# Optimization experiments

Measured on AMD Instinct MI355X. Metric: run time of the kernel, lower is better.

The kernel has to match this reference:

```python
import jax, jax.numpy as jnp
import numpy as np

N_NODES = 50000
N_EDGES = 600000
D_IN = 128
H = D_IN // 2  # 64
N_GRAPHS = 500
DIM_TARGET = 1


def setup_inputs() -> dict:
    key = jax.random.key(0)
    ks = jax.random.split(key, 16)
    x = jax.random.normal(ks[0], (N_NODES, D_IN), dtype=jnp.float32)
    edge_index = jax.random.randint(ks[1], (2, N_EDGES), 0, N_NODES, dtype=jnp.int64)
    batch = jnp.sort(jax.random.randint(ks[2], (N_NODES,), 0, N_GRAPHS, dtype=jnp.int64))
    # SAGEConv params: lin_l (neighbor aggregate, with bias), lin_r (root, no bias)
    s = 1.0 / np.sqrt(D_IN)
    Wl = jax.random.uniform(ks[3], (D_IN, H), jnp.float32, -s, s)
    bl = jnp.zeros((H,), jnp.float32)
    Wr = jax.random.uniform(ks[4], (D_IN, H), jnp.float32, -s, s)
    # MLP: 64->32->16->8->1
    dims = [H, H // 2, H // 4, H // 8, DIM_TARGET]
    params = {}
    for i in range(4):
        si = 1.0 / np.sqrt(dims[i])
        params[f"W{i}"] = jax.random.uniform(ks[5 + 2 * i], (dims[i], dims[i + 1]), jnp.float32, -si, si)
        params[f"b{i}"] = jax.random.uniform(ks[6 + 2 * i], (dims[i + 1],), jnp.float32, -si, si)
    return dict(x=x, edge_index=edge_index, batch=batch, Wl=Wl, bl=bl, Wr=Wr, **params)


def reference(x, edge_index, batch, Wl, bl, Wr, W0, b0, W1, b1, W2, b2, W3, b3):
    n_nodes = x.shape[0]
    src, dst = edge_index[0], edge_index[1]
    # SAGEConv mean aggregation: mean of source-node features at each target node
    agg = jax.ops.segment_sum(x[src], dst, num_segments=n_nodes)          # [N, D]
    cnt = jax.ops.segment_sum(jnp.ones((src.shape[0],), x.dtype), dst, num_segments=n_nodes)
    mean_nbr = agg / jnp.maximum(cnt, 1.0)[:, None]
    x1 = mean_nbr @ Wl + bl + x @ Wr                                      # [N, H]
    # global_mean_pool by graph id
    gsum = jax.ops.segment_sum(x1, batch, num_segments=N_GRAPHS)          # [G, H]
    gcnt = jax.ops.segment_sum(jnp.ones((n_nodes,), x.dtype), batch, num_segments=N_GRAPHS)
    h = gsum / jnp.maximum(gcnt, 1.0)[:, None]
    # MLP (dropout is identity in eval mode)
    h = jax.nn.relu(h @ W0 + b0)
    h = jax.nn.relu(h @ W1 + b1)
    h = jax.nn.relu(h @ W2 + b2)
    return h @ W3 + b3
```

## Files before the change

kernel.cpp:

```cpp
#include <hip/hip_runtime.h>
#include <hip/hip_bf16.h>

#define N_NODES  50000
#define N_EDGES  600000
#define D_IN     128
#define H        64
#define N_GRAPHS 500
#define MAXDEG   48

#define CONV_BLOCKS 6250
#define SCAT_CHUNKS 64
#define SCAT_BLOCKS 512
#define EDGES_PER_CHUNK (N_EDGES / SCAT_CHUNKS)
#define NODES_PER_SHARD (N_NODES / 8)
#define GST_BLOCKS  2
#define SPLIT       8

__device__ __forceinline__ float bflo(unsigned int u) { return __uint_as_float(u << 16); }
__device__ __forceinline__ float bfhi(unsigned int u) { return __uint_as_float(u & 0xffff0000u); }

__global__ __launch_bounds__(256) void prep_kernel(
        const float* __restrict__ x, unsigned short* __restrict__ xb,
        const int* __restrict__ src, const int* __restrict__ dst,
        int* __restrict__ deg, unsigned short* __restrict__ col,
        const int* __restrict__ batch, int* __restrict__ gstart) {
    int bid = blockIdx.x;
    if (bid < CONV_BLOCKS) {
        int i = bid * 256 + threadIdx.x;
        float4 f = ((const float4*)x)[i];
        ushort4 u;
        u.x = __bfloat16_as_ushort(__float2bfloat16(f.x));
        u.y = __bfloat16_as_ushort(__float2bfloat16(f.y));
        u.z = __bfloat16_as_ushort(__float2bfloat16(f.z));
        u.w = __bfloat16_as_ushort(__float2bfloat16(f.w));
        ((ushort4*)xb)[i] = u;
    } else if (bid < CONV_BLOCKS + SCAT_BLOCKS) {
        int rel   = bid - CONV_BLOCKS;
        int shard = bid & 7;
        int chunk = rel >> 3;
        int lo = shard * NODES_PER_SHARD;
        int hi = lo + NODES_PER_SHARD;
        int e0 = chunk * EDGES_PER_CHUNK;
        int e1 = e0 + EDGES_PER_CHUNK;
        for (int e = e0 + threadIdx.x; e < e1; e += 256) {
            int d = dst[e];
            if (d >= lo && d < hi) {
                int pos = atomicAdd(&deg[d], 1);
                if (pos < MAXDEG)
                    col[(size_t)d * MAXDEG + pos] = (unsigned short)src[e];
            }
        }
    } else {
        int g = (bid - CONV_BLOCKS - SCAT_BLOCKS) * 256 + threadIdx.x;
        if (g <= N_GRAPHS) {
            int lo = 0, hi = N_NODES;
            while (lo < hi) {
                int m = (lo + hi) >> 1;
                if (batch[m] < g) lo = m + 1; else hi = m;
            }
            gstart[g] = lo;
        }
    }
}

__global__ __launch_bounds__(256) void gather_kernel(
        const unsigned short* __restrict__ xb, const unsigned short* __restrict__ col,
        const int* __restrict__ deg, const int* __restrict__ batch,
        const int* __restrict__ gstart,
        float* __restrict__ Pn, float* __restrict__ Px, int* __restrict__ gcnt) {
    __shared__ float red[4 * D_IN];
    int bid  = blockIdx.x;
    int wave = threadIdx.x >> 6;
    int lane = threadIdx.x & 63;

    if (bid < N_GRAPHS * SPLIT) {
        int g = bid >> 3;
        int s = bid & 7;
        int n0 = gstart[g], n1 = gstart[g + 1];
        const unsigned short* xl = xb + 2 * lane;

        float2 pn = make_float2(0.f, 0.f);
        for (int n = n0 + s * 4 + wave; n < n1; n += 4 * SPLIT) {
            int d = deg[n];
            int dl = (d < MAXDEG) ? d : MAXDEG;
            const unsigned short* cl = col + (size_t)n * MAXDEG;
            int cidx = (lane < dl) ? (int)cl[lane] : 0;

            float2 t = make_float2(0.f, 0.f);
            int j = 0;
            for (; j + 8 <= dl; j += 8) {
                int s0 = __shfl(cidx, j),     s1 = __shfl(cidx, j + 1);
                int s2 = __shfl(cidx, j + 2), s3 = __shfl(cidx, j + 3);
                int s4 = __shfl(cidx, j + 4), s5 = __shfl(cidx, j + 5);
                int s6 = __shfl(cidx, j + 6), s7 = __shfl(cidx, j + 7);
                unsigned int u0 = *(const unsigned int*)(xl + (size_t)s0 * D_IN);
                unsigned int u1 = *(const unsigned int*)(xl + (size_t)s1 * D_IN);
                unsigned int u2 = *(const unsigned int*)(xl + (size_t)s2 * D_IN);
                unsigned int u3 = *(const unsigned int*)(xl + (size_t)s3 * D_IN);
                unsigned int u4 = *(const unsigned int*)(xl + (size_t)s4 * D_IN);
                unsigned int u5 = *(const unsigned int*)(xl + (size_t)s5 * D_IN);
                unsigned int u6 = *(const unsigned int*)(xl + (size_t)s6 * D_IN);
                unsigned int u7 = *(const unsigned int*)(xl + (size_t)s7 * D_IN);
                t.x += bflo(u0) + bflo(u1) + bflo(u2) + bflo(u3)
                     + bflo(u4) + bflo(u5) + bflo(u6) + bflo(u7);
                t.y += bfhi(u0) + bfhi(u1) + bfhi(u2) + bfhi(u3)
                     + bfhi(u4) + bfhi(u5) + bfhi(u6) + bfhi(u7);
            }
            for (; j + 4 <= dl; j += 4) {
                int s0 = __shfl(cidx, j),     s1 = __shfl(cidx, j + 1);
                int s2 = __shfl(cidx, j + 2), s3 = __shfl(cidx, j + 3);
                unsigned int u0 = *(const unsigned int*)(xl + (size_t)s0 * D_IN);
                unsigned int u1 = *(const unsigned int*)(xl + (size_t)s1 * D_IN);
                unsigned int u2 = *(const unsigned int*)(xl + (size_t)s2 * D_IN);
                unsigned int u3 = *(const unsigned int*)(xl + (size_t)s3 * D_IN);
                t.x += bflo(u0) + bflo(u1) + bflo(u2) + bflo(u3);
                t.y += bfhi(u0) + bfhi(u1) + bfhi(u2) + bfhi(u3);
            }
            for (; j < dl; ++j) {
                int sn = __shfl(cidx, j);
                unsigned int u = *(const unsigned int*)(xl + (size_t)sn * D_IN);
                t.x += bflo(u); t.y += bfhi(u);
            }
            if (d > 0) {
                float w = __builtin_amdgcn_rcpf((float)d);
                pn.x = fmaf(t.x, w, pn.x);
                pn.y = fmaf(t.y, w, pn.y);
            }
        }
        red[wave * D_IN + 2 * lane]     = pn.x;
        red[wave * D_IN + 2 * lane + 1] = pn.y;
        __syncthreads();
        if (threadIdx.x < D_IN) {
            float v = red[threadIdx.x] + red[D_IN + threadIdx.x]
                    + red[2 * D_IN + threadIdx.x] + red[3 * D_IN + threadIdx.x];
            atomicAdd(&Pn[g * D_IN + threadIdx.x], v);
        }
    } else {
        int p  = bid - N_GRAPHS * SPLIT;
        int n0 = gstart[p], n1 = gstart[p + 1];
        float fx = 0.f, fy = 0.f;
        for (int n = n0 + wave; n < n1; n += 4) {
            unsigned int u = *(const unsigned int*)(xb + (size_t)n * D_IN + 2 * lane);
            fx += bflo(u); fy += bfhi(u);
        }
        red[wave * D_IN + 2 * lane]     = fx;
        red[wave * D_IN + 2 * lane + 1] = fy;
        __syncthreads();
        if (threadIdx.x < D_IN) {
            float v = red[threadIdx.x] + red[D_IN + threadIdx.x]
                    + red[2 * D_IN + threadIdx.x] + red[3 * D_IN + threadIdx.x];
            Px[p * D_IN + threadIdx.x] = v;
        }
        if (threadIdx.x == 0) gcnt[p] = n1 - n0;
    }
}

__global__ void final_kernel(
        const float* __restrict__ Pn, const float* __restrict__ Px,
        const int* __restrict__ gcnt,
        const float* __restrict__ Wl, const float* __restrict__ bl,
        const float* __restrict__ Wr,
        const float* __restrict__ W0, const float* __restrict__ b0,
        const float* __restrict__ W1, const float* __restrict__ b1,
        const float* __restrict__ W2, const float* __restrict__ b2,
        const float* __restrict__ W3, const float* __restrict__ b3,
        float* __restrict__ out) {
    int g = blockIdx.x;
    int t = threadIdx.x;
    __shared__ float sp[D_IN], sx[D_IN], h[H], a0[32], a1[16], a2[8];
    sp[t]      = Pn[g * D_IN + t];
    sp[t + 64] = Pn[g * D_IN + 64 + t];
    sx[t]      = Px[g * D_IN + t];
    sx[t + 64] = Px[g * D_IN + 64 + t];
    __syncthreads();

    int ng = gcnt[g];
    float acc = 0.f;
    #pragma unroll 8
    for (int d = 0; d < D_IN; ++d)
        acc += sp[d] * Wl[d * H + t] + sx[d] * Wr[d * H + t];
    h[t] = (ng > 0) ? (acc / (float)ng + bl[t]) : 0.f;
    __syncthreads();

    if (t < 32) { float a = b0[t]; for (int d = 0; d < H;  ++d) a += h[d]  * W0[d * 32 + t]; a0[t] = fmaxf(a, 0.f); }
    __syncthreads();
    if (t < 16) { float a = b1[t]; for (int d = 0; d < 32; ++d) a += a0[d] * W1[d * 16 + t]; a1[t] = fmaxf(a, 0.f); }
    __syncthreads();
    if (t < 8)  { float a = b2[t]; for (int d = 0; d < 16; ++d) a += a1[d] * W2[d * 8 + t];  a2[t] = fmaxf(a, 0.f); }
    __syncthreads();
    if (t == 0) { float a = b3[0]; for (int d = 0; d < 8;  ++d) a += a2[d] * W3[d]; out[g] = a; }
}

extern "C" void kernel_launch(void* const* d_in, const int* in_sizes, int n_in,
                              void* d_out, int out_size, void* d_ws, size_t ws_size,
                              hipStream_t stream) {
    const float* x     = (const float*)d_in[0];
    const int*   ei    = (const int*)  d_in[1];
    const int*   batch = (const int*)  d_in[2];
    const float* Wl    = (const float*)d_in[3];
    const float* bl    = (const float*)d_in[4];
    const float* Wr    = (const float*)d_in[5];
    const float* W0    = (const float*)d_in[6];
    const float* b0    = (const float*)d_in[7];
    const float* W1    = (const float*)d_in[8];
    const float* b1    = (const float*)d_in[9];
    const float* W2    = (const float*)d_in[10];
    const float* b2    = (const float*)d_in[11];
    const float* W3    = (const float*)d_in[12];
    const float* b3    = (const float*)d_in[13];
    float* out = (float*)d_out;

    char* ws = (char*)d_ws;
    int*            deg    = (int*)(ws + 0);
    float*          Pn     = (float*)(ws + 200704);
    float*          Px     = (float*)(ws + 460800);
    int*            gcnt   = (int*)(ws + 716800);
    int*            gstart = (int*)(ws + 720896);
    unsigned short* col    = (unsigned short*)(ws + 724992);
    unsigned short* xb     = (unsigned short*)(ws + 5524992);

    hipMemsetAsync(ws, 0, 456704, stream);

    prep_kernel<<<CONV_BLOCKS + SCAT_BLOCKS + GST_BLOCKS, 256, 0, stream>>>(
        x, xb, ei, ei + N_EDGES, deg, col, batch, gstart);
    gather_kernel<<<N_GRAPHS * SPLIT + N_GRAPHS, 256, 0, stream>>>(
        xb, col, deg, batch, gstart, Pn, Px, gcnt);
    final_kernel<<<N_GRAPHS, 64, 0, stream>>>(Pn, Px, gcnt, Wl, bl, Wr,
                                              W0, b0, W1, b1, W2, b2, W3, b3, out);
}
```

Before: 180.7 us.

## Shard bf16 features into 8 column slices for cache-local neighbor gathers

The bf16 copy of x is reorganised into 8 contiguous slices of 16 features each, so every gather block touches only a 0.8 MB slice that can stay resident in L2. Each wave now gathers 8 neighbors at once, with 8 lanes per neighbor reading 32 bytes. Partial sums are combined with cross-lane shuffles. The grid grows to 8 slices times 4 sub-splits per graph, and the edge scatter uses more, smaller chunks. In exchange there are more blocks and atomics, and each neighbor row is loaded as short 32-byte segments rather than full rows.

```diff
diff --git a/kernel.cpp b/kernel.cpp
--- a/kernel.cpp
+++ b/kernel.cpp
@@ -8,41 +8,56 @@
 #define N_GRAPHS 500
 #define MAXDEG   48
 
-#define CONV_BLOCKS 6250
-#define SCAT_CHUNKS 64
-#define SCAT_BLOCKS 512
-#define EDGES_PER_CHUNK (N_EDGES / SCAT_CHUNKS)
-#define NODES_PER_SHARD (N_NODES / 8)
+#define NSH      8
+#define SLICE_U  (N_NODES * 8)
+
+#define CONV_BLOCKS 1563
+#define SCAT_CHUNKS 512
+#define SCAT_BLOCKS (SCAT_CHUNKS * 8)
+#define EPC         1172
+#define NPS         (N_NODES / 8)
 #define GST_BLOCKS  2
-#define SPLIT       8
+
+#define GSUB   4
+#define GMAIN  (N_GRAPHS * 8 * GSUB)
+#define PX_BLK (N_GRAPHS * 8)
 
 __device__ __forceinline__ float bflo(unsigned int u) { return __uint_as_float(u << 16); }
 __device__ __forceinline__ float bfhi(unsigned int u) { return __uint_as_float(u & 0xffff0000u); }
+__device__ __forceinline__ unsigned int packbf(float lo, float hi) {
+    unsigned int a = __bfloat16_as_ushort(__float2bfloat16(lo));
+    unsigned int b = __bfloat16_as_ushort(__float2bfloat16(hi));
+    return a | (b << 16);
+}
 
 __global__ __launch_bounds__(256) void prep_kernel(
-        const float* __restrict__ x, unsigned short* __restrict__ xb,
+        const float* __restrict__ x, unsigned int* __restrict__ xbs,
         const int* __restrict__ src, const int* __restrict__ dst,
         int* __restrict__ deg, unsigned short* __restrict__ col,
         const int* __restrict__ batch, int* __restrict__ gstart) {
-    int bid = blockIdx.x;
+    int bid = blockIdx.x, t = threadIdx.x;
     if (bid < CONV_BLOCKS) {
-        int i = bid * 256 + threadIdx.x;
-        float4 f = ((const float4*)x)[i];
-        ushort4 u;
-        u.x = __bfloat16_as_ushort(__float2bfloat16(f.x));
-        u.y = __bfloat16_as_ushort(__float2bfloat16(f.y));
-        u.z = __bfloat16_as_ushort(__float2bfloat16(f.z));
-        u.w = __bfloat16_as_ushort(__float2bfloat16(f.w));
-        ((ushort4*)xb)[i] = u;
+        int i = bid * 256 + t;
+        if (i < N_NODES * NSH) {
+            int node = i >> 3, s = i & 7;
+            const float4* xr = (const float4*)(x + (size_t)node * D_IN + s * 16);
+            float4 a = xr[0], b = xr[1], c = xr[2], d = xr[3];
+            uint4 o0, o1;
+            o0.x = packbf(a.x, a.y); o0.y = packbf(a.z, a.w);
+            o0.z = packbf(b.x, b.y); o0.w = packbf(b.z, b.w);
+            o1.x = packbf(c.x, c.y); o1.y = packbf(c.z, c.w);
+            o1.z = packbf(d.x, d.y); o1.w = packbf(d.z, d.w);
+            uint4* o = (uint4*)(xbs + (size_t)s * SLICE_U + node * 8);
+            o[0] = o0; o[1] = o1;
+        }
     } else if (bid < CONV_BLOCKS + SCAT_BLOCKS) {
         int rel   = bid - CONV_BLOCKS;
         int shard = bid & 7;
         int chunk = rel >> 3;
-        int lo = shard * NODES_PER_SHARD;
-        int hi = lo + NODES_PER_SHARD;
-        int e0 = chunk * EDGES_PER_CHUNK;
-        int e1 = e0 + EDGES_PER_CHUNK;
-        for (int e = e0 + threadIdx.x; e < e1; e += 256) {
+        int lo = shard * NPS, hi = lo + NPS;
+        int e0 = chunk * EPC;
+        int e1 = e0 + EPC; if (e1 > N_EDGES) e1 = N_EDGES;
+        for (int e = e0 + t; e < e1; e += 256) {
             int d = dst[e];
             if (d >= lo && d < hi) {
                 int pos = atomicAdd(&deg[d], 1);
@@ -51,7 +66,7 @@
             }
         }
     } else {
-        int g = (bid - CONV_BLOCKS - SCAT_BLOCKS) * 256 + threadIdx.x;
+        int g = (bid - CONV_BLOCKS - SCAT_BLOCKS) * 256 + t;
         if (g <= N_GRAPHS) {
             int lo = 0, hi = N_NODES;
             while (lo < hi) {
@@ -64,94 +79,68 @@
 }
 
 __global__ __launch_bounds__(256) void gather_kernel(
-        const unsigned short* __restrict__ xb, const unsigned short* __restrict__ col,
-        const int* __restrict__ deg, const int* __restrict__ batch,
-        const int* __restrict__ gstart,
+        const unsigned int* __restrict__ xbs, const unsigned short* __restrict__ col,
+        const int* __restrict__ deg, const int* __restrict__ gstart,
         float* __restrict__ Pn, float* __restrict__ Px, int* __restrict__ gcnt) {
-    __shared__ float red[4 * D_IN];
-    int bid  = blockIdx.x;
-    int wave = threadIdx.x >> 6;
-    int lane = threadIdx.x & 63;
-
-    if (bid < N_GRAPHS * SPLIT) {
-        int g = bid >> 3;
-        int s = bid & 7;
+    __shared__ float red[512];
+    int bid = blockIdx.x, t = threadIdx.x;
+    int wave = t >> 6, lane = t & 63;
+    int s  = bid & 7;
+    int sw = lane >> 3, pr = lane & 7;
+    const unsigned int* xs = xbs + (size_t)s * SLICE_U;
+
+    if (bid < GMAIN) {
+        int gi  = bid >> 3;
+        int g   = gi >> 2;
+        int sub = gi & 3;
         int n0 = gstart[g], n1 = gstart[g + 1];
-        const unsigned short* xl = xb + 2 * lane;
-
-        float2 pn = make_float2(0.f, 0.f);
-        for (int n = n0 + s * 4 + wave; n < n1; n += 4 * SPLIT) {
-            int d = deg[n];
+
+        float ax = 0.f, ay = 0.f;
+        for (int n = n0 + sub * 4 + wave; n < n1; n += 4 * GSUB) {
+            int d  = deg[n];
             int dl = (d < MAXDEG) ? d : MAXDEG;
-            const unsigned short* cl = col + (size_t)n * MAXDEG;
-            int cidx = (lane < dl) ? (int)cl[lane] : 0;
-
-            float2 t = make_float2(0.f, 0.f);
-            int j = 0;
-            for (; j + 8 <= dl; j += 8) {
-                int s0 = __shfl(cidx, j),     s1 = __shfl(cidx, j + 1);
-                int s2 = __shfl(cidx, j + 2), s3 = __shfl(cidx, j + 3);
-                int s4 = __shfl(cidx, j + 4), s5 = __shfl(cidx, j + 5);
-                int s6 = __shfl(cidx, j + 6), s7 = __shfl(cidx, j + 7);
-                unsigned int u0 = *(const unsigned int*)(xl + (size_t)s0 * D_IN);
-                unsigned int u1 = *(const unsigned int*)(xl + (size_t)s1 * D_IN);
-                unsigned int u2 = *(const unsigned int*)(xl + (size_t)s2 * D_IN);
-                unsigned int u3 = *(const unsigned int*)(xl + (size_t)s3 * D_IN);
-                unsigned int u4 = *(const unsigned int*)(xl + (size_t)s4 * D_IN);
-                unsigned int u5 = *(const unsigned int*)(xl + (size_t)s5 * D_IN);
-                unsigned int u6 = *(const unsigned int*)(xl + (size_t)s6 * D_IN);
-                unsigned int u7 = *(const unsigned int*)(xl + (size_t)s7 * D_IN);
-                t.x += bflo(u0) + bflo(u1) + bflo(u2) + bflo(u3)
-                     + bflo(u4) + bflo(u5) + bflo(u6) + bflo(u7);
-                t.y += bfhi(u0) + bfhi(u1) + bfhi(u2) + bfhi(u3)
-                     + bfhi(u4) + bfhi(u5) + bfhi(u6) + bfhi(u7);
-            }
-            for (; j + 4 <= dl; j += 4) {
-                int s0 = __shfl(cidx, j),     s1 = __shfl(cidx, j + 1);
-                int s2 = __shfl(cidx, j + 2), s3 = __shfl(cidx, j + 3);
-                unsigned int u0 = *(const unsigned int*)(xl + (size_t)s0 * D_IN);
-                unsigned int u1 = *(const unsigned int*)(xl + (size_t)s1 * D_IN);
-                unsigned int u2 = *(const unsigned int*)(xl + (size_t)s2 * D_IN);
-                unsigned int u3 = *(const unsigned int*)(xl + (size_t)s3 * D_IN);
-                t.x += bflo(u0) + bflo(u1) + bflo(u2) + bflo(u3);
-                t.y += bfhi(u0) + bfhi(u1) + bfhi(u2) + bfhi(u3);
-            }
-            for (; j < dl; ++j) {
-                int sn = __shfl(cidx, j);
-                unsigned int u = *(const unsigned int*)(xl + (size_t)sn * D_IN);
-                t.x += bflo(u); t.y += bfhi(u);
+            int cidx = (lane < dl) ? (int)col[(size_t)n * MAXDEG + lane] : 0;
+            float tx = 0.f, ty = 0.f;
+            for (int j = sw; j < dl; j += 8) {
+                int nb = __shfl(cidx, j);
+                unsigned int u = xs[nb * 8 + pr];
+                tx += bflo(u); ty += bfhi(u);
             }
             if (d > 0) {
                 float w = __builtin_amdgcn_rcpf((float)d);
-                pn.x = fmaf(t.x, w, pn.x);
-                pn.y = fmaf(t.y, w, pn.y);
-            }
-        }
-        red[wave * D_IN + 2 * lane]     = pn.x;
-        red[wave * D_IN + 2 * lane + 1] = pn.y;
+                ax = fmaf(tx, w, ax);
+                ay = fmaf(ty, w, ay);
+            }
+        }
+        ax += __shfl_xor(ax, 8); ax += __shfl_xor(ax, 16); ax += __shfl_xor(ax, 32);
+        ay += __shfl_xor(ay, 8); ay += __shfl_xor(ay, 16); ay += __shfl_xor(ay, 32);
+        if (lane < 8) { red[wave * 16 + 2 * pr] = ax; red[wave * 16 + 2 * pr + 1] = ay; }
         __syncthreads();
-        if (threadIdx.x < D_IN) {
-            float v = red[threadIdx.x] + red[D_IN + threadIdx.x]
-                    + red[2 * D_IN + threadIdx.x] + red[3 * D_IN + threadIdx.x];
-            atomicAdd(&Pn[g * D_IN + threadIdx.x], v);
+        if (t < 16) {
+            float v = red[t] + red[16 + t] + red[32 + t] + red[48 + t];
+            atomicAdd(&Pn[(size_t)g * D_IN + s * 16 + t], v);
         }
     } else {
-        int p  = bid - N_GRAPHS * SPLIT;
+        int p  = (bid - GMAIN) >> 3;
         int n0 = gstart[p], n1 = gstart[p + 1];
         float fx = 0.f, fy = 0.f;
-        for (int n = n0 + wave; n < n1; n += 4) {
-            unsigned int u = *(const unsigned int*)(xb + (size_t)n * D_IN + 2 * lane);
+        for (int n = n0 + (t >> 3); n < n1; n += 32) {
+            unsigned int u = xs[n * 8 + pr];
             fx += bflo(u); fy += bfhi(u);
         }
-        red[wave * D_IN + 2 * lane]     = fx;
-        red[wave * D_IN + 2 * lane + 1] = fy;
+        red[t] = fx; red[256 + t] = fy;
         __syncthreads();
-        if (threadIdx.x < D_IN) {
-            float v = red[threadIdx.x] + red[D_IN + threadIdx.x]
-                    + red[2 * D_IN + threadIdx.x] + red[3 * D_IN + threadIdx.x];
-            Px[p * D_IN + threadIdx.x] = v;
-        }
-        if (threadIdx.x == 0) gcnt[p] = n1 - n0;
+        if (t < 8) {
+            float v = 0.f;
+            for (int i = t; i < 256; i += 8) v += red[i];
+            Px[(size_t)p * D_IN + s * 16 + 2 * t] = v;
+        } else if (t < 16) {
+            int q = t - 8;
+            float v = 0.f;
+            for (int i = q; i < 256; i += 8) v += red[256 + i];
+            Px[(size_t)p * D_IN + s * 16 + 2 * q + 1] = v;
+        }
+        if (s == 0 && t == 0) gcnt[p] = n1 - n0;
     }
 }
 
@@ -213,18 +202,18 @@
     char* ws = (char*)d_ws;
     int*            deg    = (int*)(ws + 0);
     float*          Pn     = (float*)(ws + 200704);
-    float*          Px     = (float*)(ws + 460800);
-    int*            gcnt   = (int*)(ws + 716800);
-    int*            gstart = (int*)(ws + 720896);
-    unsigned short* col    = (unsigned short*)(ws + 724992);
-    unsigned short* xb     = (unsigned short*)(ws + 5524992);
+    int*            gstart = (int*)(ws + 458752);
+    unsigned short* col    = (unsigned short*)(ws + 460800);
+    unsigned int*   xbs    = (unsigned int*)(ws + 5261312);
+    float*          Px     = (float*)(ws + 18062336);
+    int*            gcnt   = (int*)(ws + 18318336);
 
     hipMemsetAsync(ws, 0, 456704, stream);
 
     prep_kernel<<<CONV_BLOCKS + SCAT_BLOCKS + GST_BLOCKS, 256, 0, stream>>>(
-        x, xb, ei, ei + N_EDGES, deg, col, batch, gstart);
-    gather_kernel<<<N_GRAPHS * SPLIT + N_GRAPHS, 256, 0, stream>>>(
-        xb, col, deg, batch, gstart, Pn, Px, gcnt);
+        x, xbs, ei, ei + N_EDGES, deg, col, batch, gstart);
+    gather_kernel<<<GMAIN + PX_BLK, 256, 0, stream>>>(
+        xbs, col, deg, gstart, Pn, Px, gcnt);
     final_kernel<<<N_GRAPHS, 64, 0, stream>>>(Pn, Px, gcnt, Wl, bl, Wr,
                                               W0, b0, W1, b1, W2, b2, W3, b3, out);
 }
```

After: 216.4 us. +19.8%, slower.

## Fuse prep, gather and MLP into one persistent kernel with grid barriers

Applied to the files above, without the earlier changes.

Replaces the memset plus three launches with a single 768-block persistent kernel. Stages are separated by atomic-counter grid barriers: zeroing the workspace, bf16 conversion and CSR scatter, per-graph gather, then the per-graph MLP. The root-feature sum now happens in the same wave loop as the neighbour gather, and partial sums go to global memory through per-lane atomics instead of a shared-memory reduction. This removes launch gaps and tail effects, but it relies on all 768 blocks being co-resident so the spin barriers do not deadlock, and it reduces parallelism in the conversion and scatter phases.

```diff
diff --git a/kernel.cpp b/kernel.cpp
--- a/kernel.cpp
+++ b/kernel.cpp
@@ -8,41 +8,92 @@
 #define N_GRAPHS 500
 #define MAXDEG   48
 
-#define CONV_BLOCKS 6250
-#define SCAT_CHUNKS 64
-#define SCAT_BLOCKS 512
-#define EDGES_PER_CHUNK (N_EDGES / SCAT_CHUNKS)
-#define NODES_PER_SHARD (N_NODES / 8)
-#define GST_BLOCKS  2
-#define SPLIT       8
+#define NBLK 768
+#define NTHR 256
+#define NW   (NBLK * NTHR)
+
+#define SCHUNKS 96
+#define EPC     (N_EDGES / SCHUNKS)
+#define NPS     (N_NODES / 8)
+
+#define GSUB   6
+#define GWAVES (N_GRAPHS * GSUB)
+
+#define OF_CTR  0
+#define OF_DEG  64
+#define OF_PN   200704
+#define OF_PX   456704
+#define OF_GST  712704
+#define OF_COL  716800
+#define OF_XB   5516800
+#define ZERO_Q  44540
 
 __device__ __forceinline__ float bflo(unsigned int u) { return __uint_as_float(u << 16); }
 __device__ __forceinline__ float bfhi(unsigned int u) { return __uint_as_float(u & 0xffff0000u); }
 
-__global__ __launch_bounds__(256) void prep_kernel(
-        const float* __restrict__ x, unsigned short* __restrict__ xb,
-        const int* __restrict__ src, const int* __restrict__ dst,
-        int* __restrict__ deg, unsigned short* __restrict__ col,
-        const int* __restrict__ batch, int* __restrict__ gstart) {
-    int bid = blockIdx.x;
-    if (bid < CONV_BLOCKS) {
-        int i = bid * 256 + threadIdx.x;
-        float4 f = ((const float4*)x)[i];
-        ushort4 u;
-        u.x = __bfloat16_as_ushort(__float2bfloat16(f.x));
-        u.y = __bfloat16_as_ushort(__float2bfloat16(f.y));
-        u.z = __bfloat16_as_ushort(__float2bfloat16(f.z));
-        u.w = __bfloat16_as_ushort(__float2bfloat16(f.w));
-        ((ushort4*)xb)[i] = u;
-    } else if (bid < CONV_BLOCKS + SCAT_BLOCKS) {
-        int rel   = bid - CONV_BLOCKS;
+__device__ __forceinline__ void gbar(int* ctr, int idx) {
+    __syncthreads();
+    if (threadIdx.x == 0) {
+        __threadfence();
+        __hip_atomic_fetch_add(&ctr[idx], 1, __ATOMIC_ACQ_REL, __HIP_MEMORY_SCOPE_AGENT);
+        while (__hip_atomic_load(&ctr[idx], __ATOMIC_ACQUIRE, __HIP_MEMORY_SCOPE_AGENT) < NBLK)
+            __builtin_amdgcn_s_sleep(1);
+        __threadfence();
+    }
+    __syncthreads();
+}
+
+__global__ __launch_bounds__(NTHR, 4) void gnn_kernel(
+        const float* __restrict__ x, const int* __restrict__ ei,
+        const int* __restrict__ batch,
+        const float* __restrict__ Wl, const float* __restrict__ bl,
+        const float* __restrict__ Wr,
+        const float* __restrict__ W0, const float* __restrict__ b0,
+        const float* __restrict__ W1, const float* __restrict__ b1,
+        const float* __restrict__ W2, const float* __restrict__ b2,
+        const float* __restrict__ W3, const float* __restrict__ b3,
+        char* __restrict__ ws, float* __restrict__ out) {
+    int* ctr             = (int*)(ws + OF_CTR);
+    int* deg             = (int*)(ws + OF_DEG);
+    float* Pn            = (float*)(ws + OF_PN);
+    float* Px            = (float*)(ws + OF_PX);
+    int* gstart          = (int*)(ws + OF_GST);
+    unsigned short* col  = (unsigned short*)(ws + OF_COL);
+    unsigned short* xb   = (unsigned short*)(ws + OF_XB);
+
+    int bid  = blockIdx.x, t = threadIdx.x;
+    int gtid = bid * NTHR + t;
+    int wave = t >> 6, lane = t & 63;
+
+    __shared__ float sp[D_IN], sx[D_IN], hs[H], a0[32], a1[16], a2[8];
+
+    const int* src = ei;
+    const int* dst = ei + N_EDGES;
+
+    {
+        uint4 z = make_uint4(0, 0, 0, 0);
+        uint4* zp = (uint4*)(ws + OF_DEG);
+        for (int i = gtid; i < ZERO_Q; i += NW) zp[i] = z;
+    }
+    gbar(ctr, 0);
+
+    {
+        const float4* xi = (const float4*)x;
+        ushort4* xo = (ushort4*)xb;
+        for (int i = gtid; i < N_NODES * D_IN / 4; i += NW) {
+            float4 f = xi[i];
+            ushort4 u;
+            u.x = __bfloat16_as_ushort(__float2bfloat16(f.x));
+            u.y = __bfloat16_as_ushort(__float2bfloat16(f.y));
+            u.z = __bfloat16_as_ushort(__float2bfloat16(f.z));
+            u.w = __bfloat16_as_ushort(__float2bfloat16(f.w));
+            xo[i] = u;
+        }
         int shard = bid & 7;
-        int chunk = rel >> 3;
-        int lo = shard * NODES_PER_SHARD;
-        int hi = lo + NODES_PER_SHARD;
-        int e0 = chunk * EDGES_PER_CHUNK;
-        int e1 = e0 + EDGES_PER_CHUNK;
-        for (int e = e0 + threadIdx.x; e < e1; e += 256) {
+        int chunk = bid >> 3;
+        int lo = shard * NPS, hi = lo + NPS;
+        int e0 = chunk * EPC, e1 = e0 + EPC;
+        for (int e = e0 + t; e < e1; e += NTHR) {
             int d = dst[e];
             if (d >= lo && d < hi) {
                 int pos = atomicAdd(&deg[d], 1);
@@ -50,145 +101,105 @@
                     col[(size_t)d * MAXDEG + pos] = (unsigned short)src[e];
             }
         }
-    } else {
-        int g = (bid - CONV_BLOCKS - SCAT_BLOCKS) * 256 + threadIdx.x;
-        if (g <= N_GRAPHS) {
-            int lo = 0, hi = N_NODES;
-            while (lo < hi) {
-                int m = (lo + hi) >> 1;
-                if (batch[m] < g) lo = m + 1; else hi = m;
+        if (bid >= NBLK - 8) {
+            int g = (bid - (NBLK - 8)) * NTHR + t;
+            if (g <= N_GRAPHS) {
+                int l = 0, h2 = N_NODES;
+                while (l < h2) { int m = (l + h2) >> 1; if (batch[m] < g) l = m + 1; else h2 = m; }
+                gstart[g] = l;
             }
-            gstart[g] = lo;
-        }
-    }
-}
-
-__global__ __launch_bounds__(256) void gather_kernel(
-        const unsigned short* __restrict__ xb, const unsigned short* __restrict__ col,
-        const int* __restrict__ deg, const int* __restrict__ batch,
-        const int* __restrict__ gstart,
-        float* __restrict__ Pn, float* __restrict__ Px, int* __restrict__ gcnt) {
-    __shared__ float red[4 * D_IN];
-    int bid  = blockIdx.x;
-    int wave = threadIdx.x >> 6;
-    int lane = threadIdx.x & 63;
-
-    if (bid < N_GRAPHS * SPLIT) {
-        int g = bid >> 3;
-        int s = bid & 7;
-        int n0 = gstart[g], n1 = gstart[g + 1];
-        const unsigned short* xl = xb + 2 * lane;
-
-        float2 pn = make_float2(0.f, 0.f);
-        for (int n = n0 + s * 4 + wave; n < n1; n += 4 * SPLIT) {
-            int d = deg[n];
-            int dl = (d < MAXDEG) ? d : MAXDEG;
-            const unsigned short* cl = col + (size_t)n * MAXDEG;
-            int cidx = (lane < dl) ? (int)cl[lane] : 0;
-
-            float2 t = make_float2(0.f, 0.f);
-            int j = 0;
-            for (; j + 8 <= dl; j += 8) {
-                int s0 = __shfl(cidx, j),     s1 = __shfl(cidx, j + 1);
-                int s2 = __shfl(cidx, j + 2), s3 = __shfl(cidx, j + 3);
-                int s4 = __shfl(cidx, j + 4), s5 = __shfl(cidx, j + 5);
-                int s6 = __shfl(cidx, j + 6), s7 = __shfl(cidx, j + 7);
-                unsigned int u0 = *(const unsigned int*)(xl + (size_t)s0 * D_IN);
-                unsigned int u1 = *(const unsigned int*)(xl + (size_t)s1 * D_IN);
-                unsigned int u2 = *(const unsigned int*)(xl + (size_t)s2 * D_IN);
-                unsigned int u3 = *(const unsigned int*)(xl + (size_t)s3 * D_IN);
-                unsigned int u4 = *(const unsigned int*)(xl + (size_t)s4 * D_IN);
-                unsigned int u5 = *(const unsigned int*)(xl + (size_t)s5 * D_IN);
-                unsigned int u6 = *(const unsigned int*)(xl + (size_t)s6 * D_IN);
-                unsigned int u7 = *(const unsigned int*)(xl + (size_t)s7 * D_IN);
-                t.x += bflo(u0) + bflo(u1) + bflo(u2) + bflo(u3)
-                     + bflo(u4) + bflo(u5) + bflo(u6) + bflo(u7);
-                t.y += bfhi(u0) + bfhi(u1) + bfhi(u2) + bfhi(u3)
-                     + bfhi(u4) + bfhi(u5) + bfhi(u6) + bfhi(u7);
+        }
+    }
+    gbar(ctr, 1);
+
+    {
+        int W = bid * 4 + wave;
+        if (W < GWAVES) {
+            int g = W / GSUB;
+            int r = W - g * GSUB;
+            int n0 = gstart[g], n1 = gstart[g + 1];
+            const unsigned short* xl = xb + 2 * lane;
+
+            float pnx = 0.f, pny = 0.f, pxx = 0.f, pxy = 0.f;
+            for (int n = n0 + r; n < n1; n += GSUB) {
+                unsigned int um = *(const unsigned int*)(xl + (size_t)n * D_IN);
+                pxx += bflo(um); pxy += bfhi(um);
+
+                int d  = deg[n];
+                int dl = (d < MAXDEG) ? d : MAXDEG;
+                int cidx = (lane < dl) ? (int)col[(size_t)n * MAXDEG + lane] : 0;
+
+                float tx = 0.f, ty = 0.f;
+                int j = 0;
+                for (; j + 8 <= dl; j += 8) {
+                    int s0 = __shfl(cidx, j),     s1 = __shfl(cidx, j + 1);
+                    int s2 = __shfl(cidx, j + 2), s3 = __shfl(cidx, j + 3);
+                    int s4 = __shfl(cidx, j + 4), s5 = __shfl(cidx, j + 5);
+                    int s6 = __shfl(cidx, j + 6), s7 = __shfl(cidx, j + 7);
+                    unsigned int u0 = *(const unsigned int*)(xl + (size_t)s0 * D_IN);
+                    unsigned int u1 = *(const unsigned int*)(xl + (size_t)s1 * D_IN);
+                    unsigned int u2 = *(const unsigned int*)(xl + (size_t)s2 * D_IN);
+                    unsigned int u3 = *(const unsigned int*)(xl + (size_t)s3 * D_IN);
+                    unsigned int u4 = *(const unsigned int*)(xl + (size_t)s4 * D_IN);
+                    unsigned int u5 = *(const unsigned int*)(xl + (size_t)s5 * D_IN);
+                    unsigned int u6 = *(const unsigned int*)(xl + (size_t)s6 * D_IN);
+                    unsigned int u7 = *(const unsigned int*)(xl + (size_t)s7 * D_IN);
+                    tx += bflo(u0) + bflo(u1) + bflo(u2) + bflo(u3)
+                        + bflo(u4) + bflo(u5) + bflo(u6) + bflo(u7);
+                    ty += bfhi(u0) + bfhi(u1) + bfhi(u2) + bfhi(u3)
+                        + bfhi(u4) + bfhi(u5) + bfhi(u6) + bfhi(u7);
+                }
+                for (; j + 4 <= dl; j += 4) {
+                    int s0 = __shfl(cidx, j),     s1 = __shfl(cidx, j + 1);
+                    int s2 = __shfl(cidx, j + 2), s3 = __shfl(cidx, j + 3);
+                    unsigned int u0 = *(const unsigned int*)(xl + (size_t)s0 * D_IN);
+                    unsigned int u1 = *(const unsigned int*)(xl + (size_t)s1 * D_IN);
+                    unsigned int u2 = *(const unsigned int*)(xl + (size_t)s2 * D_IN);
+                    unsigned int u3 = *(const unsigned int*)(xl + (size_t)s3 * D_IN);
+                    tx += bflo(u0) + bflo(u1) + bflo(u2) + bflo(u3);
+                    ty += bfhi(u0) + bfhi(u1) + bfhi(u2) + bfhi(u3);
+                }
+                for (; j < dl; ++j) {
+                    int sn = __shfl(cidx, j);
+                    unsigned int u = *(const unsigned int*)(xl + (size_t)sn * D_IN);
+                    tx += bflo(u); ty += bfhi(u);
+                }
+                if (d > 0) {
+                    float w = __builtin_amdgcn_rcpf((float)d);
+                    pnx = fmaf(tx, w, pnx);
+                    pny = fmaf(ty, w, pny);
+                }
             }
-            for (; j + 4 <= dl; j += 4) {
-                int s0 = __shfl(cidx, j),     s1 = __shfl(cidx, j + 1);
-                int s2 = __shfl(cidx, j + 2), s3 = __shfl(cidx, j + 3);
-                unsigned int u0 = *(const unsigned int*)(xl + (size_t)s0 * D_IN);
-                unsigned int u1 = *(const unsigned int*)(xl + (size_t)s1 * D_IN);
-                unsigned int u2 = *(const unsigned int*)(xl + (size_t)s2 * D_IN);
-                unsigned int u3 = *(const unsigned int*)(xl + (size_t)s3 * D_IN);
-                t.x += bflo(u0) + bflo(u1) + bflo(u2) + bflo(u3);
-                t.y += bfhi(u0) + bfhi(u1) + bfhi(u2) + bfhi(u3);
-            }
-            for (; j < dl; ++j) {
-                int sn = __shfl(cidx, j);
-                unsigned int u = *(const unsigned int*)(xl + (size_t)sn * D_IN);
-                t.x += bflo(u); t.y += bfhi(u);
-            }
-            if (d > 0) {
-                float w = __builtin_amdgcn_rcpf((float)d);
-                pn.x = fmaf(t.x, w, pn.x);
-                pn.y = fmaf(t.y, w, pn.y);
-            }
-        }
-        red[wave * D_IN + 2 * lane]     = pn.x;
-        red[wave * D_IN + 2 * lane + 1] = pn.y;
-        __syncthreads();
-        if (threadIdx.x < D_IN) {
-            float v = red[threadIdx.x] + red[D_IN + threadIdx.x]
-                    + red[2 * D_IN + threadIdx.x] + red[3 * D_IN + threadIdx.x];
-            atomicAdd(&Pn[g * D_IN + threadIdx.x], v);
-        }
-    } else {
-        int p  = bid - N_GRAPHS * SPLIT;
-        int n0 = gstart[p], n1 = gstart[p + 1];
-        float fx = 0.f, fy = 0.f;
-        for (int n = n0 + wave; n < n1; n += 4) {
-            unsigned int u = *(const unsigned int*)(xb + (size_t)n * D_IN + 2 * lane);
-            fx += bflo(u); fy += bfhi(u);
-        }
-        red[wave * D_IN + 2 * lane]     = fx;
-        red[wave * D_IN + 2 * lane + 1] = fy;
-        __syncthreads();
-        if (threadIdx.x < D_IN) {
-            float v = red[threadIdx.x] + red[D_IN + threadIdx.x]
-                    + red[2 * D_IN + threadIdx.x] + red[3 * D_IN + threadIdx.x];
-            Px[p * D_IN + threadIdx.x] = v;
-        }
-        if (threadIdx.x == 0) gcnt[p] = n1 - n0;
-    }
-}
-
-__global__ void final_kernel(
-        const float* __restrict__ Pn, const float* __restrict__ Px,
-        const int* __restrict__ gcnt,
-        const float* __restrict__ Wl, const float* __restrict__ bl,
-        const float* __restrict__ Wr,
-        const float* __restrict__ W0, const float* __restrict__ b0,
-        const float* __restrict__ W1, const float* __restrict__ b1,
-        const float* __restrict__ W2, const float* __restrict__ b2,
-        const float* __restrict__ W3, const float* __restrict__ b3,
-        float* __restrict__ out) {
-    int g = blockIdx.x;
-    int t = threadIdx.x;
-    __shared__ float sp[D_IN], sx[D_IN], h[H], a0[32], a1[16], a2[8];
-    sp[t]      = Pn[g * D_IN + t];
-    sp[t + 64] = Pn[g * D_IN + 64 + t];
-    sx[t]      = Px[g * D_IN + t];
-    sx[t + 64] = Px[g * D_IN + 64 + t];
-    __syncthreads();
-
-    int ng = gcnt[g];
-    float acc = 0.f;
-    #pragma unroll 8
-    for (int d = 0; d < D_IN; ++d)
-        acc += sp[d] * Wl[d * H + t] + sx[d] * Wr[d * H + t];
-    h[t] = (ng > 0) ? (acc / (float)ng + bl[t]) : 0.f;
-    __syncthreads();
-
-    if (t < 32) { float a = b0[t]; for (int d = 0; d < H;  ++d) a += h[d]  * W0[d * 32 + t]; a0[t] = fmaxf(a, 0.f); }
-    __syncthreads();
-    if (t < 16) { float a = b1[t]; for (int d = 0; d < 32; ++d) a += a0[d] * W1[d * 16 + t]; a1[t] = fmaxf(a, 0.f); }
-    __syncthreads();
-    if (t < 8)  { float a = b2[t]; for (int d = 0; d < 16; ++d) a += a1[d] * W2[d * 8 + t];  a2[t] = fmaxf(a, 0.f); }
-    __syncthreads();
-    if (t == 0) { float a = b3[0]; for (int d = 0; d < 8;  ++d) a += a2[d] * W3[d]; out[g] = a; }
+            float* pnp = Pn + (size_t)g * D_IN + 2 * lane;
+            float* pxp = Px + (size_t)g * D_IN + 2 * lane;
+            atomicAdd(pnp,     pnx); atomicAdd(pnp + 1, pny);
+            atomicAdd(pxp,     pxx); atomicAdd(pxp + 1, pxy);
+        }
+    }
+    gbar(ctr, 2);
+
+    if (bid < N_GRAPHS) {
+        int g = bid;
+        if (t < D_IN)      sp[t] = Pn[(size_t)g * D_IN + t];
+        else               sx[t - D_IN] = Px[(size_t)g * D_IN + (t - D_IN)];
+        __syncthreads();
+        int ng = gstart[g + 1] - gstart[g];
+        if (t < H) {
+            float acc = 0.f;
+            #pragma unroll 8
+            for (int d = 0; d < D_IN; ++d)
+                acc += sp[d] * Wl[d * H + t] + sx[d] * Wr[d * H + t];
+            hs[t] = (ng > 0) ? (acc / (float)ng + bl[t]) : 0.f;
+        }
+        __syncthreads();
+        if (t < 32) { float a = b0[t]; for (int d = 0; d < H;  ++d) a += hs[d] * W0[d * 32 + t]; a0[t] = fmaxf(a, 0.f); }
+        __syncthreads();
+        if (t < 16) { float a = b1[t]; for (int d = 0; d < 32; ++d) a += a0[d] * W1[d * 16 + t]; a1[t] = fmaxf(a, 0.f); }
+        __syncthreads();
+        if (t < 8)  { float a = b2[t]; for (int d = 0; d < 16; ++d) a += a1[d] * W2[d * 8 + t];  a2[t] = fmaxf(a, 0.f); }
+        __syncthreads();
+        if (t == 0) { float a = b3[0]; for (int d = 0; d < 8;  ++d) a += a2[d] * W3[d]; out[g] = a; }
+    }
 }
 
 extern "C" void kernel_launch(void* const* d_in, const int* in_sizes, int n_in,
@@ -210,21 +221,9 @@
     const float* b3    = (const float*)d_in[13];
     float* out = (float*)d_out;
 
-    char* ws = (char*)d_ws;
-    int*            deg    = (int*)(ws + 0);
-    float*          Pn     = (float*)(ws + 200704);
-    float*          Px     = (float*)(ws + 460800);
-    int*            gcnt   = (int*)(ws + 716800);
-    int*            gstart = (int*)(ws + 720896);
-    unsigned short* col    = (unsigned short*)(ws + 724992);
-    unsigned short* xb     = (unsigned short*)(ws + 5524992);
-
-    hipMemsetAsync(ws, 0, 456704, stream);
-
-    prep_kernel<<<CONV_BLOCKS + SCAT_BLOCKS + GST_BLOCKS, 256, 0, stream>>>(
-        x, xb, ei, ei + N_EDGES, deg, col, batch, gstart);
-    gather_kernel<<<N_GRAPHS * SPLIT + N_GRAPHS, 256, 0, stream>>>(
-        xb, col, deg, batch, gstart, Pn, Px, gcnt);
-    final_kernel<<<N_GRAPHS, 64, 0, stream>>>(Pn, Px, gcnt, Wl, bl, Wr,
-                                              W0, b0, W1, b1, W2, b2, W3, b3, out);
+    hipMemsetAsync(d_ws, 0, 64, stream);
+
+    gnn_kernel<<<NBLK, NTHR, 0, stream>>>(
+        x, ei, batch, Wl, bl, Wr, W0, b0, W1, b1, W2, b2, W3, b3,
+        (char*)d_ws, out);
 }
```

Result: slower. 571.1 us (+216.1%).
